# Kernel tuning notes

Measured on AMD Instinct MI355X. Metric: run time of the kernel, lower is better.

## Reference

```python
import jax, jax.numpy as jnp
import numpy as np

N = 100000
E_RAND = 3200000
HOP = 10
IN_DIM, HID_DIM, OUT_DIM = 512, 512, 64


def setup_inputs() -> dict:
    key = jax.random.key(0)
    ks = jax.random.split(key, 8)
    # random directed edges + self loops (norm_adj(A, True) adds self loops)
    row_r = jax.random.randint(ks[0], (E_RAND,), 0, N, dtype=jnp.int32)
    col_r = jax.random.randint(ks[1], (E_RAND,), 0, N, dtype=jnp.int32)
    loops = jnp.arange(N, dtype=jnp.int32)
    row = jnp.concatenate([row_r, loops])
    col = jnp.concatenate([col_r, loops])
    # symmetric normalization: w_ij = d_i^-1/2 * d_j^-1/2 (degrees incl. self loops)
    deg = jax.ops.segment_sum(jnp.ones(row.shape[0], jnp.float32), row, num_segments=N)
    dinv = jax.lax.rsqrt(jnp.maximum(deg, 1.0))
    edge_w = dinv[row] * dinv[col]
    x = jax.random.normal(ks[2], (N, IN_DIM), dtype=jnp.float32)
    # xavier-uniform-ish params
    lim1 = np.sqrt(2.0) * np.sqrt(6.0 / (IN_DIM + HID_DIM))
    W1 = jax.random.uniform(ks[3], (IN_DIM, HID_DIM), jnp.float32, -lim1, lim1)
    b1 = jnp.zeros((HID_DIM,), jnp.float32)
    lim2 = np.sqrt(6.0 / (HID_DIM + OUT_DIM))
    W2 = jax.random.uniform(ks[4], (HID_DIM, OUT_DIM), jnp.float32, -lim2, lim2)
    b2 = jnp.zeros((OUT_DIM,), jnp.float32)
    lims = np.sqrt(6.0 / (OUT_DIM + 1))  # gain('sigmoid') == 1
    s = jax.random.uniform(ks[5], (OUT_DIM, 1), jnp.float32, -lims, lims)
    return {"x": x, "row": row, "col": col, "edge_w": edge_w,
            "W1": W1, "b1": b1, "W2": W2, "b2": b2, "s": s}


def _spmm(row, col, w, x):
    # y[i] = sum_j A[i,j] x[j]  via gather + segment-sum scatter
    return jax.ops.segment_sum(w[:, None] * x[col], row, num_segments=N)


def reference(x, row, col, edge_w, W1, b1, W2, b2, s):
    h = jax.nn.relu(x @ W1 + b1)          # [N, hid]
    h = h @ W2 + b2                        # [N, out]
    outs = [h]
    for _ in range(HOP):
        h = _spmm(row, col, edge_w, h)
        outs.append(h)
    H = jnp.stack(outs, axis=1)            # [N, hop+1, out]
    S = jax.nn.sigmoid(jnp.einsum('nko,ol->nk', H, s))  # [N, hop+1]
    return jnp.einsum('nk,nko->no', S, H)  # [N, out]
```

## Files before the change

kernel.cpp:

```cpp
#include <hip/hip_runtime.h>
#include <math.h>
#include <stdint.h>

#define GIN_DIM 512
#define GHID_DIM 512
#define GOUT_DIM 64
#define GHOP 10

typedef __attribute__((ext_vector_type(8))) short short8;
typedef __attribute__((ext_vector_type(4))) float f32x4;

__device__ __forceinline__ unsigned f2bf_bits(float f) {
  unsigned u = __float_as_uint(f);
  return (u + 0x7FFFu + ((u >> 16) & 1u)) >> 16;
}
__device__ __forceinline__ float bf2f_bits(unsigned h) { return __uint_as_float(h << 16); }
__device__ __forceinline__ int slot_sw(int r, int o) { return (o ^ r) & 7; }


__global__ void k_count(const int* __restrict__ row, int* __restrict__ cnt, int E) {
  int e = blockIdx.x * blockDim.x + threadIdx.x;
  if (e < E) atomicAdd(&cnt[row[e]], 1);
}

__global__ __launch_bounds__(256) void k_scan1(const int* __restrict__ cnt,
                                               int* __restrict__ bsum, int n) {
  __shared__ int sd[256];
  int b = blockIdx.x, t = threadIdx.x;
  int base = b * 1024 + t * 4;
  int s = 0;
#pragma unroll
  for (int j = 0; j < 4; ++j) {
    int i = base + j;
    if (i < n) s += cnt[i];
  }
  sd[t] = s;
  __syncthreads();
  for (int off = 128; off; off >>= 1) {
    if (t < off) sd[t] += sd[t + off];
    __syncthreads();
  }
  if (t == 0) bsum[b] = sd[0];
}

__global__ __launch_bounds__(128) void k_scan2(int* __restrict__ bsum, int* __restrict__ rp,
                                               int nb, int n) {
  __shared__ int sd[128];
  int t = threadIdx.x;
  int v = (t < nb) ? bsum[t] : 0;
  int incl = v;
  sd[t] = incl;
  __syncthreads();
  for (int off = 1; off < 128; off <<= 1) {
    int add = (t >= off) ? sd[t - off] : 0;
    __syncthreads();
    incl += add;
    sd[t] = incl;
    __syncthreads();
  }
  if (t < nb) bsum[t] = incl - v;
  if (t == nb - 1) rp[n] = incl;
}

__global__ __launch_bounds__(256) void k_scan3(const int* __restrict__ cnt,
                                               const int* __restrict__ bsum,
                                               int* __restrict__ rp, int* __restrict__ nxt,
                                               int n) {
  __shared__ int sd[256];
  int b = blockIdx.x, t = threadIdx.x;
  int base = b * 1024 + t * 4;
  int v[4];
  int s = 0;
#pragma unroll
  for (int j = 0; j < 4; ++j) {
    int i = base + j;
    v[j] = (i < n) ? cnt[i] : 0;
    s += v[j];
  }
  int incl = s;
  sd[t] = incl;
  __syncthreads();
  for (int off = 1; off < 256; off <<= 1) {
    int add = (t >= off) ? sd[t - off] : 0;
    __syncthreads();
    incl += add;
    sd[t] = incl;
    __syncthreads();
  }
  int run = incl - s + bsum[b];
#pragma unroll
  for (int j = 0; j < 4; ++j) {
    int i = base + j;
    if (i < n) {
      rp[i] = run;
      nxt[i] = run;
      run += v[j];
    }
  }
}

__global__ void k_scatter(const int* __restrict__ row, const int* __restrict__ col,
                          const float* __restrict__ ew, int* __restrict__ nxt,
                          int2* __restrict__ epk, int E) {
  int e = blockIdx.x * blockDim.x + threadIdx.x;
  if (e < E) {
    int r = row[e];
    int p = atomicAdd(&nxt[r], 1);
    epk[p] = make_int2(col[e], __float_as_int(ew[e]));
  }
}


__global__ __launch_bounds__(1024) void k_w1t(const float* __restrict__ w1,
                                              ushort* __restrict__ hi,
                                              ushort* __restrict__ lo) {
  __shared__ float t[32][33];
  int bx = blockIdx.x;
  int by = blockIdx.y;
  int tx = threadIdx.x & 31, ty = threadIdx.x >> 5;
  t[ty][tx] = w1[(size_t)(by * 32 + ty) * GHID_DIM + bx * 32 + tx];
  __syncthreads();
  float v = t[tx][ty];
  unsigned h = f2bf_bits(v);
  unsigned l = f2bf_bits(v - bf2f_bits(h));
  size_t o = (size_t)(bx * 32 + ty) * GIN_DIM + by * 32 + tx;
  hi[o] = (ushort)h;
  lo[o] = (ushort)l;
}


__global__ __launch_bounds__(256) void k_gemm1(const float* __restrict__ x,
                                               const ushort* __restrict__ w1h,
                                               const ushort* __restrict__ w1l,
                                               const float* __restrict__ b1,
                                               float* __restrict__ h, int n, int cbase) {
  __shared__ __align__(16) ushort Ah[128 * 64];
  __shared__ __align__(16) ushort Al[128 * 64];
  __shared__ __align__(16) ushort Bh[128 * 64];
  __shared__ __align__(16) ushort Bl[128 * 64];
  int tid = threadIdx.x;
  int wave = tid >> 6, lane = tid & 63;
  int wm = wave >> 1, wn = wave & 1;
  int fr = lane & 15, fq = lane >> 4;
  int rowbase = blockIdx.x * 128;

  f32x4 acc[4][4];
#pragma unroll
  for (int m = 0; m < 4; ++m)
#pragma unroll
    for (int q = 0; q < 4; ++q) acc[m][q] = (f32x4)(0.f);

  int sr = tid >> 1;
  int sk = (tid & 1) * 32;

  for (int ks = 0; ks < GIN_DIM; ks += 64) {
    {
      int gr = rowbase + sr;
      float vals[32];
      if (gr < n) {
        const float* px = x + (size_t)gr * GIN_DIM + ks + sk;
#pragma unroll
        for (int q = 0; q < 8; ++q) {
          float4 v = *(const float4*)(px + q * 4);
          vals[q * 4 + 0] = v.x;
          vals[q * 4 + 1] = v.y;
          vals[q * 4 + 2] = v.z;
          vals[q * 4 + 3] = v.w;
        }
      } else {
#pragma unroll
        for (int q = 0; q < 32; ++q) vals[q] = 0.f;
      }
#pragma unroll
      for (int o4 = 0; o4 < 4; ++o4) {
        short8 vh, vl;
#pragma unroll
        for (int j = 0; j < 8; ++j) {
          float a = vals[o4 * 8 + j];
          unsigned hb = f2bf_bits(a);
          float r = a - bf2f_bits(hb);
          unsigned lb = f2bf_bits(r);
          vh[j] = (short)hb;
          vl[j] = (short)lb;
        }
        int oct = (sk >> 3) + o4;
        int off = sr * 64 + slot_sw(sr, oct) * 8;
        *reinterpret_cast<short8*>(&Ah[off]) = vh;
        *reinterpret_cast<short8*>(&Al[off]) = vl;
      }
    }
    {
      const ushort* ph = w1h + (size_t)(cbase + sr) * GIN_DIM + ks + sk;
      const ushort* pl = w1l + (size_t)(cbase + sr) * GIN_DIM + ks + sk;
#pragma unroll
      for (int o4 = 0; o4 < 4; ++o4) {
        short8 vh = *reinterpret_cast<const short8*>(ph + o4 * 8);
        short8 vl = *reinterpret_cast<const short8*>(pl + o4 * 8);
        int oct = (sk >> 3) + o4;
        int off = sr * 64 + slot_sw(sr, oct) * 8;
        *reinterpret_cast<short8*>(&Bh[off]) = vh;
        *reinterpret_cast<short8*>(&Bl[off]) = vl;
      }
    }
    __syncthreads();

#pragma unroll
    for (int kk = 0; kk < 2; ++kk) {
      int koct = kk * 4 + fq;
      short8 bH[4], bL[4];
#pragma unroll
      for (int q = 0; q < 4; ++q) {
        int c = wn * 64 + q * 16 + fr;
        int off = c * 64 + slot_sw(c, koct) * 8;
        bH[q] = *reinterpret_cast<const short8*>(&Bh[off]);
        bL[q] = *reinterpret_cast<const short8*>(&Bl[off]);
      }
#pragma unroll
      for (int m = 0; m < 4; ++m) {
        int r = wm * 64 + m * 16 + fr;
        int off = r * 64 + slot_sw(r, koct) * 8;
        short8 aH = *reinterpret_cast<const short8*>(&Ah[off]);
        short8 aL = *reinterpret_cast<const short8*>(&Al[off]);
#pragma unroll
        for (int q = 0; q < 4; ++q) {
          f32x4 t = acc[m][q];
          t = __builtin_amdgcn_mfma_f32_16x16x32_bf16(aH, bL[q], t, 0, 0, 0);
          t = __builtin_amdgcn_mfma_f32_16x16x32_bf16(aL, bH[q], t, 0, 0, 0);
          t = __builtin_amdgcn_mfma_f32_16x16x32_bf16(aH, bH[q], t, 0, 0, 0);
          acc[m][q] = t;
        }
      }
    }
    __syncthreads();
  }

#pragma unroll
  for (int m = 0; m < 4; ++m) {
#pragma unroll
    for (int q = 0; q < 4; ++q) {
      int coll = wn * 64 + q * 16 + fr;
      float bias = b1[cbase + coll];
#pragma unroll
      for (int j = 0; j < 4; ++j) {
        int rowl = wm * 64 + m * 16 + fq * 4 + j;
        int grow = rowbase + rowl;
        if (grow < n) h[(size_t)grow * 128 + coll] = fmaxf(acc[m][q][j] + bias, 0.f);
      }
    }
  }
}


__global__ __launch_bounds__(256) void k_gemm2(const float* __restrict__ h,
                                               const float* __restrict__ w2,
                                               const float* __restrict__ b2,
                                               float* __restrict__ plane, int n, int cbase,
                                               int first) {
  __shared__ float hs[64][132];
  __shared__ float w2s[128][64];
  int tid = threadIdx.x;
  int rowbase = blockIdx.x * 64;
  {
    int r = tid >> 2, q = (tid & 3) * 32;
    int g = rowbase + r;
    if (g < n) {
      const float* ph = h + (size_t)g * 128 + q;
#pragma unroll
      for (int i = 0; i < 8; ++i) *(float4*)&hs[r][q + i * 4] = *(const float4*)(ph + i * 4);
    } else {
#pragma unroll
      for (int i = 0; i < 32; ++i) hs[r][q + i] = 0.f;
    }
    int k = tid >> 1, half = (tid & 1) * 32;
    const float* pw = w2 + (size_t)(cbase + k) * GOUT_DIM + half;
#pragma unroll
    for (int i = 0; i < 8; ++i) *(float4*)&w2s[k][half + i * 4] = *(const float4*)(pw + i * 4);
  }
  __syncthreads();

  int trow = tid >> 2, tc = (tid & 3) * 16;
  float acc[16] = {};
  for (int k = 0; k < 128; ++k) {
    float hv = hs[trow][k];
#pragma unroll
    for (int j4 = 0; j4 < 4; ++j4) {
      float4 w = *(const float4*)&w2s[k][tc + j4 * 4];
      acc[j4 * 4 + 0] = fmaf(hv, w.x, acc[j4 * 4 + 0]);
      acc[j4 * 4 + 1] = fmaf(hv, w.y, acc[j4 * 4 + 1]);
      acc[j4 * 4 + 2] = fmaf(hv, w.z, acc[j4 * 4 + 2]);
      acc[j4 * 4 + 3] = fmaf(hv, w.w, acc[j4 * 4 + 3]);
    }
  }
  int g = rowbase + trow;
  if (g < n) {
    float* pp = plane + (size_t)g * GOUT_DIM + tc;
    if (first) {
#pragma unroll
      for (int j4 = 0; j4 < 4; ++j4) {
        float4 b = *(const float4*)&b2[tc + j4 * 4];
        float4 o = make_float4(acc[j4 * 4 + 0] + b.x, acc[j4 * 4 + 1] + b.y,
                               acc[j4 * 4 + 2] + b.z, acc[j4 * 4 + 3] + b.w);
        *(float4*)(pp + j4 * 4) = o;
      }
    } else {
#pragma unroll
      for (int j4 = 0; j4 < 4; ++j4) {
        float4 o = *(const float4*)(pp + j4 * 4);
        o.x += acc[j4 * 4 + 0];
        o.y += acc[j4 * 4 + 1];
        o.z += acc[j4 * 4 + 2];
        o.w += acc[j4 * 4 + 3];
        *(float4*)(pp + j4 * 4) = o;
      }
    }
  }
}


__global__ void k_combine(const float* __restrict__ h0, const float* __restrict__ s,
                          float* __restrict__ out, int n) {
  int wave = (int)((blockIdx.x * blockDim.x + threadIdx.x) >> 6);
  int lane = threadIdx.x & 63;
  if (wave >= n) return;
  float v = h0[(size_t)wave * GOUT_DIM + lane];
  float dot = v * s[lane];
#pragma unroll
  for (int off = 32; off; off >>= 1) dot += __shfl_xor(dot, off);
  float sig = 1.f / (1.f + __expf(-dot));
  out[(size_t)wave * GOUT_DIM + lane] = sig * v;
}


__global__ void k_spmm(const int* __restrict__ rp, const int2* __restrict__ epk,
                       const float* __restrict__ hin, float* __restrict__ hout,
                       const float* __restrict__ s, float* __restrict__ out, int n) {
  int wave = (int)((blockIdx.x * blockDim.x + threadIdx.x) >> 6);
  int lane = threadIdx.x & 63;
  if (wave >= n) return;
  int e0 = __builtin_amdgcn_readfirstlane(rp[wave]);
  int e1 = __builtin_amdgcn_readfirstlane(rp[wave + 1]);
  float sl = s[lane];
  float acc = 0.f, acc2 = 0.f;
  int e = e0;
  for (; e + 4 <= e1; e += 4) {
    int2 p0 = epk[e], p1 = epk[e + 1], p2 = epk[e + 2], p3 = epk[e + 3];
    float v0 = hin[(size_t)p0.x * GOUT_DIM + lane];
    float v1 = hin[(size_t)p1.x * GOUT_DIM + lane];
    float v2 = hin[(size_t)p2.x * GOUT_DIM + lane];
    float v3 = hin[(size_t)p3.x * GOUT_DIM + lane];
    acc = fmaf(__int_as_float(p0.y), v0, acc);
    acc2 = fmaf(__int_as_float(p1.y), v1, acc2);
    acc = fmaf(__int_as_float(p2.y), v2, acc);
    acc2 = fmaf(__int_as_float(p3.y), v3, acc2);
  }
  for (; e < e1; ++e) {
    int2 p = epk[e];
    acc = fmaf(__int_as_float(p.y), hin[(size_t)p.x * GOUT_DIM + lane], acc);
  }
  acc += acc2;
  hout[(size_t)wave * GOUT_DIM + lane] = acc;
  float dot = acc * sl;
#pragma unroll
  for (int off = 32; off; off >>= 1) dot += __shfl_xor(dot, off);
  float sig = 1.f / (1.f + __expf(-dot));
  out[(size_t)wave * GOUT_DIM + lane] += sig * acc;
}


static inline char* align256(char* p) {
  return (char*)(((uintptr_t)p + 255) & ~(uintptr_t)255);
}

extern "C" void kernel_launch(void* const* d_in, const int* in_sizes, int n_in,
                              void* d_out, int out_size, void* d_ws, size_t ws_size,
                              hipStream_t stream) {
  const float* x = (const float*)d_in[0];
  const int* row = (const int*)d_in[1];
  const int* col = (const int*)d_in[2];
  const float* ew = (const float*)d_in[3];
  const float* W1 = (const float*)d_in[4];
  const float* b1 = (const float*)d_in[5];
  const float* W2 = (const float*)d_in[6];
  const float* b2 = (const float*)d_in[7];
  const float* s = (const float*)d_in[8];
  float* out = (float*)d_out;

  int N = in_sizes[0] / GIN_DIM;
  int E = in_sizes[1];

  char* w = (char*)d_ws;
  float* h_chunk = (float*)w; w = align256(w + (size_t)N * 128 * sizeof(float));
  float* planeA = (float*)w;  w = align256(w + (size_t)N * GOUT_DIM * sizeof(float));
  float* planeB = (float*)w;  w = align256(w + (size_t)N * GOUT_DIM * sizeof(float));
  int* cnt = (int*)w;         w = align256(w + (size_t)N * sizeof(int));
  int* rp = (int*)w;          w = align256(w + ((size_t)N + 1) * sizeof(int));
  int* nxt = (int*)w;         w = align256(w + (size_t)N * sizeof(int));
  int* bsum = (int*)w;        w = align256(w + 256 * sizeof(int));
  int2* epk = (int2*)w;       w = align256(w + (size_t)E * sizeof(int2));
  ushort* w1h = (ushort*)w;   w = align256(w + (size_t)GIN_DIM * GHID_DIM * sizeof(ushort));
  ushort* w1l = (ushort*)w;   w = align256(w + (size_t)GIN_DIM * GHID_DIM * sizeof(ushort));

  int nb = (N + 1023) / 1024;

  hipMemsetAsync(cnt, 0, (size_t)N * sizeof(int), stream);
  k_count<<<(E + 255) / 256, 256, 0, stream>>>(row, cnt, E);
  k_scan1<<<nb, 256, 0, stream>>>(cnt, bsum, N);
  k_scan2<<<1, 128, 0, stream>>>(bsum, rp, nb, N);
  k_scan3<<<nb, 256, 0, stream>>>(cnt, bsum, rp, nxt, N);
  k_scatter<<<(E + 255) / 256, 256, 0, stream>>>(row, col, ew, nxt, epk, E);

  k_w1t<<<dim3(16, 16), 1024, 0, stream>>>(W1, w1h, w1l);

  for (int c = 0; c < 4; ++c) {
    k_gemm1<<<(N + 127) / 128, 256, 0, stream>>>(x, w1h, w1l, b1, h_chunk, N, c * 128);
    k_gemm2<<<(N + 63) / 64, 256, 0, stream>>>(h_chunk, W2, b2, planeA, N, c * 128, c == 0);
  }

  k_combine<<<(N + 3) / 4, 256, 0, stream>>>(planeA, s, out, N);

  const float* hin = planeA;
  float* hout = planeB;
  for (int k = 0; k < GHOP; ++k) {
    k_spmm<<<(N + 3) / 4, 256, 0, stream>>>(rp, epk, hin, hout, s, out, N);
    float* t = (float*)hin;
    hin = hout;
    hout = t;
  }
}
```

Baseline: 2.365 ms.

## Fuse both dense GEMMs into one kernel, slice CSR build atomics, unroll SpMM

The two-layer MLP becomes a single kernel. The hidden chunk stays in LDS as split-bf16 and is multiplied by W2 through MFMA, which removes the h_chunk round trip through global memory and the separate FP32 GEMM2 launches. The count and scatter kernels now partition rows into 8 slices by block, so the atomics in each pass hit a narrower address range, at the cost of reading the row array 8 times. The SpMM inner loop is unrolled to 8 edges with 4 accumulators and a predicated tail. The fused kernel recomputes nothing, but it serialises W2 staging inside the block and may lower occupancy.

```diff
diff --git a/kernel.cpp b/kernel.cpp
--- a/kernel.cpp
+++ b/kernel.cpp
@@ -6,6 +6,7 @@
 #define GHID_DIM 512
 #define GOUT_DIM 64
 #define GHOP 10
+#define NSLICE 8
 
 typedef __attribute__((ext_vector_type(8))) short short8;
 typedef __attribute__((ext_vector_type(4))) float f32x4;
@@ -18,9 +19,28 @@
 __device__ __forceinline__ int slot_sw(int r, int o) { return (o ^ r) & 7; }
 
 
-__global__ void k_count(const int* __restrict__ row, int* __restrict__ cnt, int E) {
-  int e = blockIdx.x * blockDim.x + threadIdx.x;
-  if (e < E) atomicAdd(&cnt[row[e]], 1);
+__global__ __launch_bounds__(256) void k_count(const int* __restrict__ row, int* __restrict__ cnt,
+                                               int E, float sliceScale) {
+  int slice = blockIdx.x & (NSLICE - 1);
+  int base = ((blockIdx.x >> 3) * 256 + threadIdx.x) * 4;
+  if (base + 3 < E) {
+    int4 r4 = *(const int4*)(row + base);
+    int rr[4] = {r4.x, r4.y, r4.z, r4.w};
+#pragma unroll
+    for (int j = 0; j < 4; ++j) {
+      int sl = min(NSLICE - 1, (int)((float)rr[j] * sliceScale));
+      if (sl == slice) atomicAdd(&cnt[rr[j]], 1);
+    }
+  } else {
+    for (int j = 0; j < 4; ++j) {
+      int e = base + j;
+      if (e < E) {
+        int r = row[e];
+        int sl = min(NSLICE - 1, (int)((float)r * sliceScale));
+        if (sl == slice) atomicAdd(&cnt[r], 1);
+      }
+    }
+  }
 }
 
 __global__ __launch_bounds__(256) void k_scan1(const int* __restrict__ cnt,
@@ -99,14 +119,37 @@
   }
 }
 
-__global__ void k_scatter(const int* __restrict__ row, const int* __restrict__ col,
-                          const float* __restrict__ ew, int* __restrict__ nxt,
-                          int2* __restrict__ epk, int E) {
-  int e = blockIdx.x * blockDim.x + threadIdx.x;
-  if (e < E) {
-    int r = row[e];
-    int p = atomicAdd(&nxt[r], 1);
-    epk[p] = make_int2(col[e], __float_as_int(ew[e]));
+__global__ __launch_bounds__(256) void k_scatter(const int* __restrict__ row,
+                                                 const int* __restrict__ col,
+                                                 const float* __restrict__ ew,
+                                                 int* __restrict__ nxt, int2* __restrict__ epk,
+                                                 int E, float sliceScale) {
+  int slice = blockIdx.x & (NSLICE - 1);
+  int base = ((blockIdx.x >> 3) * 256 + threadIdx.x) * 4;
+  if (base + 3 < E) {
+    int4 r4 = *(const int4*)(row + base);
+    int rr[4] = {r4.x, r4.y, r4.z, r4.w};
+#pragma unroll
+    for (int j = 0; j < 4; ++j) {
+      int sl = min(NSLICE - 1, (int)((float)rr[j] * sliceScale));
+      if (sl == slice) {
+        int e = base + j;
+        int p = atomicAdd(&nxt[rr[j]], 1);
+        epk[p] = make_int2(col[e], __float_as_int(ew[e]));
+      }
+    }
+  } else {
+    for (int j = 0; j < 4; ++j) {
+      int e = base + j;
+      if (e < E) {
+        int r = row[e];
+        int sl = min(NSLICE - 1, (int)((float)r * sliceScale));
+        if (sl == slice) {
+          int p = atomicAdd(&nxt[r], 1);
+          epk[p] = make_int2(col[e], __float_as_int(ew[e]));
+        }
+      }
+    }
   }
 }
 
@@ -129,11 +172,10 @@
 }
 
 
-__global__ __launch_bounds__(256) void k_gemm1(const float* __restrict__ x,
-                                               const ushort* __restrict__ w1h,
-                                               const ushort* __restrict__ w1l,
-                                               const float* __restrict__ b1,
-                                               float* __restrict__ h, int n, int cbase) {
+__global__ __launch_bounds__(256, 2) void k_dense(
+    const float* __restrict__ x, const ushort* __restrict__ w1h, const ushort* __restrict__ w1l,
+    const float* __restrict__ b1, const float* __restrict__ w2, const float* __restrict__ b2,
+    float* __restrict__ plane, int n) {
   __shared__ __align__(16) ushort Ah[128 * 64];
   __shared__ __align__(16) ushort Al[128 * 64];
   __shared__ __align__(16) ushort Bh[128 * 64];
@@ -143,177 +185,193 @@
   int wm = wave >> 1, wn = wave & 1;
   int fr = lane & 15, fq = lane >> 4;
   int rowbase = blockIdx.x * 128;
-
-  f32x4 acc[4][4];
-#pragma unroll
-  for (int m = 0; m < 4; ++m)
-#pragma unroll
-    for (int q = 0; q < 4; ++q) acc[m][q] = (f32x4)(0.f);
-
   int sr = tid >> 1;
   int sk = (tid & 1) * 32;
 
-  for (int ks = 0; ks < GIN_DIM; ks += 64) {
-    {
-      int gr = rowbase + sr;
-      float vals[32];
-      if (gr < n) {
-        const float* px = x + (size_t)gr * GIN_DIM + ks + sk;
-#pragma unroll
-        for (int q = 0; q < 8; ++q) {
-          float4 v = *(const float4*)(px + q * 4);
-          vals[q * 4 + 0] = v.x;
-          vals[q * 4 + 1] = v.y;
-          vals[q * 4 + 2] = v.z;
-          vals[q * 4 + 3] = v.w;
-        }
+  f32x4 acc2[2][4];
+#pragma unroll
+  for (int m2 = 0; m2 < 2; ++m2)
+#pragma unroll
+    for (int q2 = 0; q2 < 4; ++q2) {
+      float bv = b2[q2 * 16 + fr];
+      acc2[m2][q2] = (f32x4)(bv);
+    }
+
+  for (int c = 0; c < 4; ++c) {
+    int cbase = c * 128;
+    f32x4 acc[4][4];
+#pragma unroll
+    for (int m = 0; m < 4; ++m)
+#pragma unroll
+      for (int q = 0; q < 4; ++q) acc[m][q] = (f32x4)(0.f);
+
+    for (int ks = 0; ks < GIN_DIM; ks += 64) {
+      {
+        int gr = rowbase + sr;
+        float vals[32];
+        if (gr < n) {
+          const float* px = x + (size_t)gr * GIN_DIM + ks + sk;
+#pragma unroll
+          for (int q = 0; q < 8; ++q) {
+            float4 v = *(const float4*)(px + q * 4);
+            vals[q * 4 + 0] = v.x;
+            vals[q * 4 + 1] = v.y;
+            vals[q * 4 + 2] = v.z;
+            vals[q * 4 + 3] = v.w;
+          }
+        } else {
+#pragma unroll
+          for (int q = 0; q < 32; ++q) vals[q] = 0.f;
+        }
+#pragma unroll
+        for (int o4 = 0; o4 < 4; ++o4) {
+          short8 vh, vl;
+#pragma unroll
+          for (int j = 0; j < 8; ++j) {
+            float a = vals[o4 * 8 + j];
+            unsigned hb = f2bf_bits(a);
+            float r = a - bf2f_bits(hb);
+            unsigned lb = f2bf_bits(r);
+            vh[j] = (short)hb;
+            vl[j] = (short)lb;
+          }
+          int oct = (sk >> 3) + o4;
+          int off = sr * 64 + slot_sw(sr, oct) * 8;
+          *reinterpret_cast<short8*>(&Ah[off]) = vh;
+          *reinterpret_cast<short8*>(&Al[off]) = vl;
+        }
+      }
+      {
+        const ushort* ph = w1h + (size_t)(cbase + sr) * GIN_DIM + ks + sk;
+        const ushort* pl = w1l + (size_t)(cbase + sr) * GIN_DIM + ks + sk;
+#pragma unroll
+        for (int o4 = 0; o4 < 4; ++o4) {
+          short8 vh = *reinterpret_cast<const short8*>(ph + o4 * 8);
+          short8 vl = *reinterpret_cast<const short8*>(pl + o4 * 8);
+          int oct = (sk >> 3) + o4;
+          int off = sr * 64 + slot_sw(sr, oct) * 8;
+          *reinterpret_cast<short8*>(&Bh[off]) = vh;
+          *reinterpret_cast<short8*>(&Bl[off]) = vl;
+        }
+      }
+      __syncthreads();
+#pragma unroll
+      for (int kk = 0; kk < 2; ++kk) {
+        int koct = kk * 4 + fq;
+        short8 bH[4], bL[4];
+#pragma unroll
+        for (int q = 0; q < 4; ++q) {
+          int cc = wn * 64 + q * 16 + fr;
+          int off = cc * 64 + slot_sw(cc, koct) * 8;
+          bH[q] = *reinterpret_cast<const short8*>(&Bh[off]);
+          bL[q] = *reinterpret_cast<const short8*>(&Bl[off]);
+        }
+#pragma unroll
+        for (int m = 0; m < 4; ++m) {
+          int r = wm * 64 + m * 16 + fr;
+          int off = r * 64 + slot_sw(r, koct) * 8;
+          short8 aH = *reinterpret_cast<const short8*>(&Ah[off]);
+          short8 aL = *reinterpret_cast<const short8*>(&Al[off]);
+#pragma unroll
+          for (int q = 0; q < 4; ++q) {
+            f32x4 t = acc[m][q];
+            t = __builtin_amdgcn_mfma_f32_16x16x32_bf16(aH, bL[q], t, 0, 0, 0);
+            t = __builtin_amdgcn_mfma_f32_16x16x32_bf16(aL, bH[q], t, 0, 0, 0);
+            t = __builtin_amdgcn_mfma_f32_16x16x32_bf16(aH, bH[q], t, 0, 0, 0);
+            acc[m][q] = t;
+          }
+        }
+      }
+      __syncthreads();
+    }
+
+#pragma unroll
+    for (int m = 0; m < 4; ++m)
+#pragma unroll
+      for (int q = 0; q < 4; ++q) {
+        float bias = b1[cbase + wn * 64 + q * 16 + fr];
+#pragma unroll
+        for (int j = 0; j < 4; ++j) acc[m][q][j] = fmaxf(acc[m][q][j] + bias, 0.f);
+      }
+
+#pragma unroll
+    for (int sub = 0; sub < 2; ++sub) {
+      if (wn == sub) {
+#pragma unroll
+        for (int m = 0; m < 4; ++m)
+#pragma unroll
+          for (int q = 0; q < 4; ++q) {
+            int colq = q * 16 + fr;
+            int oct = colq >> 3;
+#pragma unroll
+            for (int j = 0; j < 4; ++j) {
+              int r = wm * 64 + m * 16 + fq * 4 + j;
+              float v = acc[m][q][j];
+              unsigned hb = f2bf_bits(v);
+              unsigned lb = f2bf_bits(v - bf2f_bits(hb));
+              int off = r * 64 + slot_sw(r, oct) * 8 + (colq & 7);
+              Ah[off] = (ushort)hb;
+              Al[off] = (ushort)lb;
+            }
+          }
       } else {
-#pragma unroll
-        for (int q = 0; q < 32; ++q) vals[q] = 0.f;
-      }
-#pragma unroll
-      for (int o4 = 0; o4 < 4; ++o4) {
-        short8 vh, vl;
-#pragma unroll
-        for (int j = 0; j < 8; ++j) {
-          float a = vals[o4 * 8 + j];
-          unsigned hb = f2bf_bits(a);
-          float r = a - bf2f_bits(hb);
-          unsigned lb = f2bf_bits(r);
-          vh[j] = (short)hb;
-          vl[j] = (short)lb;
-        }
-        int oct = (sk >> 3) + o4;
-        int off = sr * 64 + slot_sw(sr, oct) * 8;
-        *reinterpret_cast<short8*>(&Ah[off]) = vh;
-        *reinterpret_cast<short8*>(&Al[off]) = vl;
-      }
-    }
-    {
-      const ushort* ph = w1h + (size_t)(cbase + sr) * GIN_DIM + ks + sk;
-      const ushort* pl = w1l + (size_t)(cbase + sr) * GIN_DIM + ks + sk;
-#pragma unroll
-      for (int o4 = 0; o4 < 4; ++o4) {
-        short8 vh = *reinterpret_cast<const short8*>(ph + o4 * 8);
-        short8 vl = *reinterpret_cast<const short8*>(pl + o4 * 8);
-        int oct = (sk >> 3) + o4;
-        int off = sr * 64 + slot_sw(sr, oct) * 8;
-        *reinterpret_cast<short8*>(&Bh[off]) = vh;
-        *reinterpret_cast<short8*>(&Bl[off]) = vl;
-      }
-    }
-    __syncthreads();
-
-#pragma unroll
-    for (int kk = 0; kk < 2; ++kk) {
-      int koct = kk * 4 + fq;
-      short8 bH[4], bL[4];
-#pragma unroll
-      for (int q = 0; q < 4; ++q) {
-        int c = wn * 64 + q * 16 + fr;
-        int off = c * 64 + slot_sw(c, koct) * 8;
-        bH[q] = *reinterpret_cast<const short8*>(&Bh[off]);
-        bL[q] = *reinterpret_cast<const short8*>(&Bl[off]);
-      }
-#pragma unroll
-      for (int m = 0; m < 4; ++m) {
-        int r = wm * 64 + m * 16 + fr;
-        int off = r * 64 + slot_sw(r, koct) * 8;
-        short8 aH = *reinterpret_cast<const short8*>(&Ah[off]);
-        short8 aL = *reinterpret_cast<const short8*>(&Al[off]);
-#pragma unroll
-        for (int q = 0; q < 4; ++q) {
-          f32x4 t = acc[m][q];
-          t = __builtin_amdgcn_mfma_f32_16x16x32_bf16(aH, bL[q], t, 0, 0, 0);
-          t = __builtin_amdgcn_mfma_f32_16x16x32_bf16(aL, bH[q], t, 0, 0, 0);
-          t = __builtin_amdgcn_mfma_f32_16x16x32_bf16(aH, bH[q], t, 0, 0, 0);
-          acc[m][q] = t;
-        }
-      }
-    }
-    __syncthreads();
-  }
-
-#pragma unroll
-  for (int m = 0; m < 4; ++m) {
-#pragma unroll
-    for (int q = 0; q < 4; ++q) {
-      int coll = wn * 64 + q * 16 + fr;
-      float bias = b1[cbase + coll];
+        int t2 = wm * 64 + lane;
+        int oc = t2 >> 1;
+        int k0 = (t2 & 1) * 32;
+#pragma unroll
+        for (int i = 0; i < 32; ++i) {
+          int k = k0 + i;
+          float v = w2[(size_t)(cbase + sub * 64 + k) * GOUT_DIM + oc];
+          unsigned hb = f2bf_bits(v);
+          unsigned lb = f2bf_bits(v - bf2f_bits(hb));
+          int off = oc * 64 + slot_sw(oc, k >> 3) * 8 + (k & 7);
+          Bh[off] = (ushort)hb;
+          Bl[off] = (ushort)lb;
+        }
+      }
+      __syncthreads();
+#pragma unroll
+      for (int kk = 0; kk < 2; ++kk) {
+        int koct = kk * 4 + fq;
+        short8 bH[4], bL[4];
+#pragma unroll
+        for (int q2 = 0; q2 < 4; ++q2) {
+          int c2 = q2 * 16 + fr;
+          int off = c2 * 64 + slot_sw(c2, koct) * 8;
+          bH[q2] = *reinterpret_cast<const short8*>(&Bh[off]);
+          bL[q2] = *reinterpret_cast<const short8*>(&Bl[off]);
+        }
+#pragma unroll
+        for (int m2 = 0; m2 < 2; ++m2) {
+          int r2 = wave * 32 + m2 * 16 + fr;
+          int off = r2 * 64 + slot_sw(r2, koct) * 8;
+          short8 aH = *reinterpret_cast<const short8*>(&Ah[off]);
+          short8 aL = *reinterpret_cast<const short8*>(&Al[off]);
+#pragma unroll
+          for (int q2 = 0; q2 < 4; ++q2) {
+            f32x4 t = acc2[m2][q2];
+            t = __builtin_amdgcn_mfma_f32_16x16x32_bf16(aH, bL[q2], t, 0, 0, 0);
+            t = __builtin_amdgcn_mfma_f32_16x16x32_bf16(aL, bH[q2], t, 0, 0, 0);
+            t = __builtin_amdgcn_mfma_f32_16x16x32_bf16(aH, bH[q2], t, 0, 0, 0);
+            acc2[m2][q2] = t;
+          }
+        }
+      }
+      __syncthreads();
+    }
+  }
+
+#pragma unroll
+  for (int m2 = 0; m2 < 2; ++m2)
+#pragma unroll
+    for (int q2 = 0; q2 < 4; ++q2) {
+      int col = q2 * 16 + fr;
 #pragma unroll
       for (int j = 0; j < 4; ++j) {
-        int rowl = wm * 64 + m * 16 + fq * 4 + j;
-        int grow = rowbase + rowl;
-        if (grow < n) h[(size_t)grow * 128 + coll] = fmaxf(acc[m][q][j] + bias, 0.f);
-      }
-    }
-  }
-}
-
-
-__global__ __launch_bounds__(256) void k_gemm2(const float* __restrict__ h,
-                                               const float* __restrict__ w2,
-                                               const float* __restrict__ b2,
-                                               float* __restrict__ plane, int n, int cbase,
-                                               int first) {
-  __shared__ float hs[64][132];
-  __shared__ float w2s[128][64];
-  int tid = threadIdx.x;
-  int rowbase = blockIdx.x * 64;
-  {
-    int r = tid >> 2, q = (tid & 3) * 32;
-    int g = rowbase + r;
-    if (g < n) {
-      const float* ph = h + (size_t)g * 128 + q;
-#pragma unroll
-      for (int i = 0; i < 8; ++i) *(float4*)&hs[r][q + i * 4] = *(const float4*)(ph + i * 4);
-    } else {
-#pragma unroll
-      for (int i = 0; i < 32; ++i) hs[r][q + i] = 0.f;
-    }
-    int k = tid >> 1, half = (tid & 1) * 32;
-    const float* pw = w2 + (size_t)(cbase + k) * GOUT_DIM + half;
-#pragma unroll
-    for (int i = 0; i < 8; ++i) *(float4*)&w2s[k][half + i * 4] = *(const float4*)(pw + i * 4);
-  }
-  __syncthreads();
-
-  int trow = tid >> 2, tc = (tid & 3) * 16;
-  float acc[16] = {};
-  for (int k = 0; k < 128; ++k) {
-    float hv = hs[trow][k];
-#pragma unroll
-    for (int j4 = 0; j4 < 4; ++j4) {
-      float4 w = *(const float4*)&w2s[k][tc + j4 * 4];
-      acc[j4 * 4 + 0] = fmaf(hv, w.x, acc[j4 * 4 + 0]);
-      acc[j4 * 4 + 1] = fmaf(hv, w.y, acc[j4 * 4 + 1]);
-      acc[j4 * 4 + 2] = fmaf(hv, w.z, acc[j4 * 4 + 2]);
-      acc[j4 * 4 + 3] = fmaf(hv, w.w, acc[j4 * 4 + 3]);
-    }
-  }
-  int g = rowbase + trow;
-  if (g < n) {
-    float* pp = plane + (size_t)g * GOUT_DIM + tc;
-    if (first) {
-#pragma unroll
-      for (int j4 = 0; j4 < 4; ++j4) {
-        float4 b = *(const float4*)&b2[tc + j4 * 4];
-        float4 o = make_float4(acc[j4 * 4 + 0] + b.x, acc[j4 * 4 + 1] + b.y,
-                               acc[j4 * 4 + 2] + b.z, acc[j4 * 4 + 3] + b.w);
-        *(float4*)(pp + j4 * 4) = o;
-      }
-    } else {
-#pragma unroll
-      for (int j4 = 0; j4 < 4; ++j4) {
-        float4 o = *(const float4*)(pp + j4 * 4);
-        o.x += acc[j4 * 4 + 0];
-        o.y += acc[j4 * 4 + 1];
-        o.z += acc[j4 * 4 + 2];
-        o.w += acc[j4 * 4 + 3];
-        *(float4*)(pp + j4 * 4) = o;
-      }
-    }
-  }
+        int grow = rowbase + wave * 32 + m2 * 16 + fq * 4 + j;
+        if (grow < n) plane[(size_t)grow * GOUT_DIM + col] = acc2[m2][q2][j];
+      }
+    }
 }
 
 
@@ -331,33 +389,56 @@
 }
 
 
-__global__ void k_spmm(const int* __restrict__ rp, const int2* __restrict__ epk,
-                       const float* __restrict__ hin, float* __restrict__ hout,
-                       const float* __restrict__ s, float* __restrict__ out, int n) {
+__global__ __launch_bounds__(256) void k_spmm(const int* __restrict__ rp,
+                                              const int2* __restrict__ epk,
+                                              const float* __restrict__ hin,
+                                              float* __restrict__ hout,
+                                              const float* __restrict__ s,
+                                              float* __restrict__ out, int n) {
   int wave = (int)((blockIdx.x * blockDim.x + threadIdx.x) >> 6);
   int lane = threadIdx.x & 63;
   if (wave >= n) return;
   int e0 = __builtin_amdgcn_readfirstlane(rp[wave]);
   int e1 = __builtin_amdgcn_readfirstlane(rp[wave + 1]);
   float sl = s[lane];
-  float acc = 0.f, acc2 = 0.f;
-  int e = e0;
-  for (; e + 4 <= e1; e += 4) {
-    int2 p0 = epk[e], p1 = epk[e + 1], p2 = epk[e + 2], p3 = epk[e + 3];
+  float a0 = 0.f, a1 = 0.f, a2 = 0.f, a3 = 0.f;
+  int em = e0 + ((e1 - e0) & ~7);
+  for (int e = e0; e < em; e += 8) {
+    int2 p0 = epk[e + 0], p1 = epk[e + 1], p2 = epk[e + 2], p3 = epk[e + 3];
+    int2 p4 = epk[e + 4], p5 = epk[e + 5], p6 = epk[e + 6], p7 = epk[e + 7];
     float v0 = hin[(size_t)p0.x * GOUT_DIM + lane];
     float v1 = hin[(size_t)p1.x * GOUT_DIM + lane];
     float v2 = hin[(size_t)p2.x * GOUT_DIM + lane];
     float v3 = hin[(size_t)p3.x * GOUT_DIM + lane];
-    acc = fmaf(__int_as_float(p0.y), v0, acc);
-    acc2 = fmaf(__int_as_float(p1.y), v1, acc2);
-    acc = fmaf(__int_as_float(p2.y), v2, acc);
-    acc2 = fmaf(__int_as_float(p3.y), v3, acc2);
-  }
-  for (; e < e1; ++e) {
-    int2 p = epk[e];
-    acc = fmaf(__int_as_float(p.y), hin[(size_t)p.x * GOUT_DIM + lane], acc);
-  }
-  acc += acc2;
+    float v4 = hin[(size_t)p4.x * GOUT_DIM + lane];
+    float v5 = hin[(size_t)p5.x * GOUT_DIM + lane];
+    float v6 = hin[(size_t)p6.x * GOUT_DIM + lane];
+    float v7 = hin[(size_t)p7.x * GOUT_DIM + lane];
+    a0 = fmaf(__int_as_float(p0.y), v0, a0);
+    a1 = fmaf(__int_as_float(p1.y), v1, a1);
+    a2 = fmaf(__int_as_float(p2.y), v2, a2);
+    a3 = fmaf(__int_as_float(p3.y), v3, a3);
+    a0 = fmaf(__int_as_float(p4.y), v4, a0);
+    a1 = fmaf(__int_as_float(p5.y), v5, a1);
+    a2 = fmaf(__int_as_float(p6.y), v6, a2);
+    a3 = fmaf(__int_as_float(p7.y), v7, a3);
+  }
+  if (em < e1) {
+    int last = e1 - 1;
+#pragma unroll
+    for (int j = 0; j < 8; ++j) {
+      int e = em + j;
+      int ec = e < last ? e : last;
+      int2 p = epk[ec];
+      float w = (e < e1) ? __int_as_float(p.y) : 0.f;
+      float v = hin[(size_t)p.x * GOUT_DIM + lane];
+      if (j & 1)
+        a1 = fmaf(w, v, a1);
+      else
+        a0 = fmaf(w, v, a0);
+    }
+  }
+  float acc = (a0 + a1) + (a2 + a3);
   hout[(size_t)wave * GOUT_DIM + lane] = acc;
   float dot = acc * sl;
 #pragma unroll
@@ -389,7 +470,6 @@
   int E = in_sizes[1];
 
   char* w = (char*)d_ws;
-  float* h_chunk = (float*)w; w = align256(w + (size_t)N * 128 * sizeof(float));
   float* planeA = (float*)w;  w = align256(w + (size_t)N * GOUT_DIM * sizeof(float));
   float* planeB = (float*)w;  w = align256(w + (size_t)N * GOUT_DIM * sizeof(float));
   int* cnt = (int*)w;         w = align256(w + (size_t)N * sizeof(int));
@@ -401,20 +481,19 @@
   ushort* w1l = (ushort*)w;   w = align256(w + (size_t)GIN_DIM * GHID_DIM * sizeof(ushort));
 
   int nb = (N + 1023) / 1024;
+  int nbe = (E + 1023) / 1024;
+  float sliceScale = (float)NSLICE / (float)N;
 
   hipMemsetAsync(cnt, 0, (size_t)N * sizeof(int), stream);
-  k_count<<<(E + 255) / 256, 256, 0, stream>>>(row, cnt, E);
+  k_count<<<nbe * NSLICE, 256, 0, stream>>>(row, cnt, E, sliceScale);
   k_scan1<<<nb, 256, 0, stream>>>(cnt, bsum, N);
   k_scan2<<<1, 128, 0, stream>>>(bsum, rp, nb, N);
   k_scan3<<<nb, 256, 0, stream>>>(cnt, bsum, rp, nxt, N);
-  k_scatter<<<(E + 255) / 256, 256, 0, stream>>>(row, col, ew, nxt, epk, E);
+  k_scatter<<<nbe * NSLICE, 256, 0, stream>>>(row, col, ew, nxt, epk, E, sliceScale);
 
   k_w1t<<<dim3(16, 16), 1024, 0, stream>>>(W1, w1h, w1l);
 
-  for (int c = 0; c < 4; ++c) {
-    k_gemm1<<<(N + 127) / 128, 256, 0, stream>>>(x, w1h, w1l, b1, h_chunk, N, c * 128);
-    k_gemm2<<<(N + 63) / 64, 256, 0, stream>>>(h_chunk, W2, b2, planeA, N, c * 128, c == 0);
-  }
+  k_dense<<<(N + 127) / 128, 256, 0, stream>>>(x, w1h, w1l, b1, W2, b2, planeA, N);
 
   k_combine<<<(N + 3) / 4, 256, 0, stream>>>(planeA, s, out, N);
 
```

Measured after the change: 2.435 ms. +3.0%, slower.
